# Optimization experiments

Hardware: AMD Instinct MI355X
Metric: run time of the kernel (lower is better)

## Reference

```python
import jax, jax.numpy as jnp
import numpy as np

C_SIZE = 512
DOWN = 8
W = C_SIZE // DOWN           # 64
REG = 10.0
N_ITER = 100                 # num_of_iter_in_ot

COOD = jnp.arange(0, C_SIZE, DOWN, dtype=jnp.float32) + DOWN / 2.0  # (W,)


def _cost_matrix(pts):
    # pts: (N,2) pixel coords -> squared L2 distance to every grid cell, (N, W*W)
    x = pts[:, 0:1]
    y = pts[:, 1:2]
    cood = COOD[None, :]
    x_dis = -2.0 * x * cood + x * x + cood * cood      # (N, W)
    y_dis = -2.0 * y * cood + y * y + cood * cood      # (N, W)
    dis = y_dis[:, :, None] + x_dis[:, None, :]        # (N, W, W): rows=y, cols=x
    return dis.reshape(pts.shape[0], -1)


def _asgd_semi_dual(a, b, M, idxs):
    # POT ot.stochastic.solve_semi_dual_entropic with method='asgd'.
    # a: (n,) target (point) weights; b: (m,) source (density) weights; M: (n, m).
    n, m = M.shape
    lr = 1.0 / jnp.max(a / REG)          # POT default lr
    log_b = jnp.log(b)

    def step(carry, xk):
        cur, ave = carry
        i, k = xk
        Mi = M[i]
        khi = jax.nn.softmax((cur - Mi) / REG + log_b)   # stable softmax
        cur = cur + (lr / jnp.sqrt(k)) * (b - khi)
        ave = cur / k + (1.0 - 1.0 / k) * ave
        return (cur, ave), None

    ks = jnp.arange(1, idxs.shape[0] + 1, dtype=jnp.float32)
    (_, beta), _ = jax.lax.scan(step, (jnp.zeros(m, M.dtype), jnp.zeros(m, M.dtype)), (idxs, ks))
    # c-transform: alpha_i = -reg * log sum_j exp((beta_j - M_ij)/reg) * b_j
    alpha = -REG * jax.scipy.special.logsumexp((beta[None, :] - M) / REG + log_b[None, :], axis=1)
    pi = jnp.exp((alpha[:, None] + beta[None, :] - M) / REG) * a[:, None] * b[None, :]
    return beta, pi


def _per_sample(normed, unnormed, pts, idxs):
    # normed, unnormed: (W, W); pts: (N, 2); idxs: (N_ITER,)
    n = pts.shape[0]
    a = jnp.full((n,), 1.0 / n, dtype=jnp.float32)
    dis = jax.lax.stop_gradient(_cost_matrix(pts))            # cupy path: no grad
    b = jax.lax.stop_gradient(normed.reshape(-1))             # src_prob detached
    beta, pi = _asgd_semi_dual(a, b, dis, idxs)
    beta = jax.lax.stop_gradient(beta)
    ot_obj = jnp.sum(normed.reshape(-1) * beta)
    src = jax.lax.stop_gradient(unnormed.reshape(-1))         # source_density detached
    sc = src.sum()
    denom = sc * sc + 1e-16
    im_grad = jax.lax.stop_gradient(sc / denom * beta - jnp.sum(src * beta) / denom)
    loss = jnp.sum(unnormed.reshape(-1) * im_grad)
    wd = jnp.sum(dis * jax.lax.stop_gradient(pi))
    return loss, wd, ot_obj


def setup_inputs() -> dict:
    key = jax.random.key(0)
    k1, k2 = jax.random.split(key, 2)
    unnormed = jax.random.uniform(k1, (16, 1, W, W), dtype=jnp.float32)
    normed = unnormed / unnormed.sum(axis=(1, 2, 3), keepdims=True)
    points = jax.random.uniform(k2, (16, 512, 2), dtype=jnp.float32) * C_SIZE
    return {"normed_density": normed, "unnormed_density": unnormed, "points": points}


def reference(normed_density, unnormed_density, points):
    B = normed_density.shape[0]
    # random coordinate indices for ASGD (constant, deterministic)
    idxs = jax.random.randint(jax.random.key(1), (B, N_ITER), 0, points.shape[1])
    loss, wd, ot_obj = jax.vmap(_per_sample)(
        normed_density[:, 0], unnormed_density[:, 0], points, idxs)
    return jnp.stack([loss.sum(), wd.sum(), ot_obj.sum()])
```

## Files before the change

### kernel.cpp

```cpp
#include <hip/hip_runtime.h>
#include <math.h>

#define NSAMP 16
#define NPTS  512
#define MDIM  4096
#define NIT   100

#define R0MAX 48


__device__ __forceinline__ int swz(int r, int c) {
  return r * 64 + (c ^ ((r & 1) << 4));
}

__device__ __forceinline__ void tf2x32(unsigned k0, unsigned k1,
                                       unsigned c0, unsigned c1,
                                       unsigned &o0, unsigned &o1)
{
  unsigned ks2 = k0 ^ k1 ^ 0x1BD11BDAu;
  unsigned x0 = c0 + k0, x1 = c1 + k1;
#define ROT(r) x0 += x1; x1 = (x1 << (r)) | (x1 >> (32 - (r))); x1 ^= x0;
#define G0 ROT(13) ROT(15) ROT(26) ROT(6)
#define G1 ROT(17) ROT(29) ROT(16) ROT(24)
  G0 x0 += k1;  x1 += ks2 + 1u;
  G1 x0 += ks2; x1 += k0  + 2u;
  G0 x0 += k0;  x1 += k1  + 3u;
  G1 x0 += k1;  x1 += ks2 + 4u;
  G0 x0 += ks2; x1 += k0  + 5u;
#undef G0
#undef G1
#undef ROT
  o0 = x0; o1 = x1;
}

__device__ __forceinline__ int rand_idx(int f)
{
  unsigned ka, kb, w0, w1;
  tf2x32(0u, 1u, 0u, 1u, ka, kb);
  tf2x32(ka, kb, 0u, (unsigned)f, w0, w1);
  return (int)((w0 ^ w1) & 511u);
}

template<int CTRL>
__device__ __forceinline__ float dpp_mv(float v, float id)
{
  return __int_as_float(__builtin_amdgcn_update_dpp(
      __float_as_int(id), __float_as_int(v), CTRL, 0xF, 0xF, false));
}

__device__ __forceinline__ float waveSum(float v)
{
  v += dpp_mv<0x111>(v, 0.0f);
  v += dpp_mv<0x112>(v, 0.0f);
  v += dpp_mv<0x114>(v, 0.0f);
  v += dpp_mv<0x118>(v, 0.0f);
  v += dpp_mv<0x142>(v, 0.0f);
  v += dpp_mv<0x143>(v, 0.0f);
  return __int_as_float(__builtin_amdgcn_readlane(__float_as_int(v), 63));
}

__global__ __launch_bounds__(1024) void kern_fused(
    const float *__restrict__ normed, const float *__restrict__ pts,
    float *__restrict__ out)
{
  const int s = blockIdx.x;
  const int t = threadIdx.x;
  const int v = t >> 6;
  const int L = t & 63;

  __shared__ float2 dav[MDIM];
  __shared__ float  barr[MDIM];
  __shared__ float2 pts2[NPTS];
  __shared__ float4 cstA[NIT + 4];
  __shared__ int2   cstB[NIT + 4];
  __shared__ float  spfin;
  __shared__ float  wdred[16], otred[16];

  #pragma unroll
  for (int l = 0; l < 4; ++l) {
    const int r = 4 * v + l;
    const float bv = normed[s * MDIM + r * 64 + L];
    const int idx = swz(r, L);
    dav[idx]  = make_float2(__logf(bv), 0.0f);
    barr[idx] = bv;
  }
  if (t < NPTS) pts2[t] = ((const float2 *)pts)[s * NPTS + t];
  if (t < NIT + 4) {
    const int kk = t < NIT ? t : (NIT - 1);
    const int idx = rand_idx(s * NIT + kk);
    const float2 p = ((const float2 *)pts)[s * NPTS + idx];
    const int rn = (int)floorf((p.y - 4.0f) * 0.125f + 0.5f);
    const int cn = (int)floorf((p.x - 4.0f) * 0.125f + 0.5f);
    int r0 = rn - 7; r0 = r0 < 0 ? 0 : (r0 > R0MAX ? R0MAX : r0);
    int c0 = cn - 7; c0 = c0 < 0 ? 0 : (c0 > R0MAX ? R0MAX : c0);
    const float kf    = (float)(kk + 1);
    const float step1 = 512.0f * __builtin_amdgcn_rsqf(kf);
    const float Pk    = step1 * (0.01f * (101.0f - kf));
    cstA[t] = make_float4(p.x - (float)(8 * c0 + 4),
                          p.y - (float)(8 * r0 + 4), step1, Pk);
    cstB[t] = make_int2(r0, c0);
  }
  __syncthreads();

  const int rbase = L >> 4;
  const int cbase = L & 15;
  const float fc8 = (float)(8 * cbase);
  const float fr8 = (float)(8 * rbase);

  if (t == 64) {
    float SPa = 0.0f;
    for (int k = 0; k < NIT; ++k) SPa += cstA[k].w;
    spfin = SPa;
  }
  if (v == 0) {
    float A = 0.0f;
    float4 cA = cstA[0];
    int2   cB = cstB[0];
    int j0 = swz(cB.x + rbase, cB.y + cbase);
    float2 c0v = dav[j0      ]; float b0v = barr[j0      ];
    float2 c1v = dav[j0 + 256]; float b1v = barr[j0 + 256];
    float2 c2v = dav[j0 + 512]; float b2v = barr[j0 + 512];
    float2 c3v = dav[j0 + 768]; float b3v = barr[j0 + 768];

    for (int k = 0; k < NIT; ++k) {
      const float4 cAn = cstA[k + 1];
      const int2   cBn = cstB[k + 1];

      const float dx  = cA.x - fc8;
      const float dxx = dx * dx;
      const float ty  = cA.y - fr8;
      const float e0 = __expf(fmaf(fmaf(ty,          ty,          dxx), -0.1f, fmaf(b0v, A, c0v.x)));
      const float e1 = __expf(fmaf(fmaf(ty - 32.0f, ty - 32.0f, dxx), -0.1f, fmaf(b1v, A, c1v.x)));
      const float e2 = __expf(fmaf(fmaf(ty - 64.0f, ty - 64.0f, dxx), -0.1f, fmaf(b2v, A, c2v.x)));
      const float e3 = __expf(fmaf(fmaf(ty - 96.0f, ty - 96.0f, dxx), -0.1f, fmaf(b3v, A, c3v.x)));

      const float S    = waveSum((e0 + e1) + (e2 + e3));
      const float invS = __builtin_amdgcn_rcpf(S);
      const float cD = cA.z * invS, cAv = cA.w * invS;

      c0v.x = fmaf(-cD, e0, c0v.x); c0v.y = fmaf(cAv, e0, c0v.y);
      c1v.x = fmaf(-cD, e1, c1v.x); c1v.y = fmaf(cAv, e1, c1v.y);
      c2v.x = fmaf(-cD, e2, c2v.x); c2v.y = fmaf(cAv, e2, c2v.y);
      c3v.x = fmaf(-cD, e3, c3v.x); c3v.y = fmaf(cAv, e3, c3v.y);
      dav[j0      ] = c0v;
      dav[j0 + 256] = c1v;
      dav[j0 + 512] = c2v;
      dav[j0 + 768] = c3v;

      A += cA.z;

      cA = cAn; cB = cBn;
      j0 = swz(cB.x + rbase, cB.y + cbase);
      c0v = dav[j0      ]; b0v = barr[j0      ];
      c1v = dav[j0 + 256]; b1v = barr[j0 + 256];
      c2v = dav[j0 + 512]; b2v = barr[j0 + 512];
      c3v = dav[j0 + 768]; b3v = barr[j0 + 768];
    }
  }
  __syncthreads();

  {
    const float SP = spfin;
    float p_ot = 0.0f;
    #pragma unroll
    for (int l = 0; l < 4; ++l) {
      const int idx = swz(4 * v + l, L);
      const float2 cd = dav[idx];
      const float bb  = barr[idx];
      const float tt  = fmaf(bb, SP, -cd.y);
      barr[idx] = tt + __logf(bb);
      p_ot = fmaf(bb, 10.0f * tt, p_ot);
    }
    p_ot = waveSum(p_ot);
    if (L == 0) otred[v] = p_ot;
  }
  __syncthreads();

  float wdacc = 0.0f;
  for (int g = 0; g < 8; ++g) {
    float pe[4], pq[4];
    #pragma unroll
    for (int i = 0; i < 4; ++i) {
      const int p = 32 * v + 4 * g + i;
      const float2 pt = pts2[p];
      const float x = pt.x, y = pt.y;
      const int rn = (int)floorf((y - 4.0f) * 0.125f + 0.5f);
      const int cn = (int)floorf((x - 4.0f) * 0.125f + 0.5f);
      int r0 = rn - 7; r0 = r0 < 0 ? 0 : (r0 > R0MAX ? R0MAX : r0);
      int c0 = cn - 7; c0 = c0 < 0 ? 0 : (c0 > R0MAX ? R0MAX : c0);
      const int rl = r0 + rbase;
      const int cl = c0 + cbase;
      const int j0 = swz(rl, cl);

      const float dx  = x - (float)(8 * cl + 4);
      const float dxx = dx * dx;
      const float ty  = y - (float)(8 * rl + 4);
      float spe = 0.0f, spq = 0.0f;
      #pragma unroll
      for (int q = 0; q < 4; ++q) {
        const float wv = barr[j0 + 256 * q];
        const float dy = ty - (float)(32 * q);
        const float qq = fmaf(dy, dy, dxx);
        const float e  = __expf(fmaf(qq, -0.1f, wv));
        spe += e;
        spq = fmaf(e, qq, spq);
      }
      pe[i] = spe; pq[i] = spq;
    }
    #pragma unroll
    for (int i = 0; i < 4; ++i) { pe[i] += dpp_mv<0x111>(pe[i], 0.0f); pq[i] += dpp_mv<0x111>(pq[i], 0.0f); }
    #pragma unroll
    for (int i = 0; i < 4; ++i) { pe[i] += dpp_mv<0x112>(pe[i], 0.0f); pq[i] += dpp_mv<0x112>(pq[i], 0.0f); }
    #pragma unroll
    for (int i = 0; i < 4; ++i) { pe[i] += dpp_mv<0x114>(pe[i], 0.0f); pq[i] += dpp_mv<0x114>(pq[i], 0.0f); }
    #pragma unroll
    for (int i = 0; i < 4; ++i) { pe[i] += dpp_mv<0x118>(pe[i], 0.0f); pq[i] += dpp_mv<0x118>(pq[i], 0.0f); }
    #pragma unroll
    for (int i = 0; i < 4; ++i) { pe[i] += dpp_mv<0x142>(pe[i], 0.0f); pq[i] += dpp_mv<0x142>(pq[i], 0.0f); }
    #pragma unroll
    for (int i = 0; i < 4; ++i) { pe[i] += dpp_mv<0x143>(pe[i], 0.0f); pq[i] += dpp_mv<0x143>(pq[i], 0.0f); }
    #pragma unroll
    for (int i = 0; i < 4; ++i) {
      const float PE = __int_as_float(__builtin_amdgcn_readlane(__float_as_int(pe[i]), 63));
      const float PQ = __int_as_float(__builtin_amdgcn_readlane(__float_as_int(pq[i]), 63));
      wdacc = fmaf(PQ, __builtin_amdgcn_rcpf(PE), wdacc);
    }
  }
  if (L == 0) wdred[v] = wdacc;
  __syncthreads();
  if (t == 0) {
    float wd = 0.0f, ot = 0.0f;
    #pragma unroll
    for (int i = 0; i < 16; ++i) { wd += wdred[i]; ot += otred[i]; }
    atomicAdd(&out[1], wd * (1.0f / 512.0f));
    atomicAdd(&out[2], ot);
  }
}

extern "C" void kernel_launch(void* const* d_in, const int* in_sizes, int n_in,
                              void* d_out, int out_size, void* d_ws, size_t ws_size,
                              hipStream_t stream)
{
  (void)in_sizes; (void)n_in; (void)out_size; (void)d_ws; (void)ws_size;
  const float *normed = (const float *)d_in[0];
  const float *pts    = (const float *)d_in[2];
  float *out = (float *)d_out;

  hipMemsetAsync(out, 0, 3 * sizeof(float), stream);
  kern_fused<<<dim3(NSAMP), dim3(1024), 0, stream>>>(normed, pts, out);
}
```

Baseline: 92.78 us.

## Batch disjoint-window ASGD iterations across waves with block barriers

Instead of running all 100 sequential ASGD updates on one wave, the kernel groups up to four consecutive iterations whose 32x32-region windows do not overlap and runs each on a separate wave. Because updates to disjoint regions commute, the batches execute in parallel with a __syncthreads between batches. A prefix-sum array of step sizes lets each wave know the running A value for its iteration. This adds a block-wide barrier per batch plus serial batch planning by one thread, which may cost more than the saved serial steps if windows often overlap.

```diff
diff --git a/kernel.cpp b/kernel.cpp
--- a/kernel.cpp
+++ b/kernel.cpp
@@ -8,9 +8,17 @@
 
 #define R0MAX 48
 
+#define MAXB 4
+
 
 __device__ __forceinline__ int swz(int r, int c) {
   return r * 64 + (c ^ ((r & 1) << 4));
+}
+
+__device__ __forceinline__ int wdisj(int2 a, int2 b) {
+  int dr = a.x - b.x; if (dr < 0) dr = -dr;
+  int dc = a.y - b.y; if (dc < 0) dc = -dc;
+  return (dr >= 16) | (dc >= 16);
 }
 
 __device__ __forceinline__ void tf2x32(unsigned k0, unsigned k1,
@@ -73,6 +81,11 @@
   __shared__ float2 pts2[NPTS];
   __shared__ float4 cstA[NIT + 4];
   __shared__ int2   cstB[NIT + 4];
+  __shared__ float  Aarr[NIT];
+  __shared__ int    lenb[NIT];
+  __shared__ int    bstart_s[NIT];
+  __shared__ int    bsize_s[NIT];
+  __shared__ int    nbat_s;
   __shared__ float  spfin;
   __shared__ float  wdred[16], otred[16];
 
@@ -102,62 +115,99 @@
   }
   __syncthreads();
 
+  if (t < NIT) {
+    const int2 w0 = cstB[t];
+    int e1 = 0, e2 = 0, e3 = 0;
+    if (t + 1 < NIT) {
+      const int2 w1 = cstB[t + 1];
+      e1 = wdisj(w0, w1);
+      if (e1 && t + 2 < NIT) {
+        const int2 w2 = cstB[t + 2];
+        e2 = wdisj(w0, w2) & wdisj(w1, w2);
+        if (e2 && t + 3 < NIT) {
+          const int2 w3 = cstB[t + 3];
+          e3 = wdisj(w0, w3) & wdisj(w1, w3) & wdisj(w2, w3);
+        }
+      }
+    }
+    lenb[t] = 1 + e1 + e2 + e3;
+  }
+  __syncthreads();
+
+  if (t == 0) {
+    int i = 0, b = 0;
+    while (i < NIT) {
+      bstart_s[b] = i;
+      const int Lb = lenb[i];
+      bsize_s[b] = Lb;
+      i += Lb;
+      ++b;
+    }
+    nbat_s = b;
+  } else if (t == 64) {
+    float A = 0.0f, SPa = 0.0f;
+    for (int k = 0; k < NIT; ++k) {
+      Aarr[k] = A;
+      A   += cstA[k].z;
+      SPa += cstA[k].w;
+    }
+    spfin = SPa;
+  }
+  __syncthreads();
+
   const int rbase = L >> 4;
   const int cbase = L & 15;
   const float fc8 = (float)(8 * cbase);
   const float fr8 = (float)(8 * rbase);
 
-  if (t == 64) {
-    float SPa = 0.0f;
-    for (int k = 0; k < NIT; ++k) SPa += cstA[k].w;
-    spfin = SPa;
-  }
-  if (v == 0) {
-    float A = 0.0f;
-    float4 cA = cstA[0];
-    int2   cB = cstB[0];
-    int j0 = swz(cB.x + rbase, cB.y + cbase);
-    float2 c0v = dav[j0      ]; float b0v = barr[j0      ];
-    float2 c1v = dav[j0 + 256]; float b1v = barr[j0 + 256];
-    float2 c2v = dav[j0 + 512]; float b2v = barr[j0 + 512];
-    float2 c3v = dav[j0 + 768]; float b3v = barr[j0 + 768];
-
-    for (int k = 0; k < NIT; ++k) {
-      const float4 cAn = cstA[k + 1];
-      const int2   cBn = cstB[k + 1];
-
-      const float dx  = cA.x - fc8;
-      const float dxx = dx * dx;
-      const float ty  = cA.y - fr8;
-      const float e0 = __expf(fmaf(fmaf(ty,          ty,          dxx), -0.1f, fmaf(b0v, A, c0v.x)));
-      const float e1 = __expf(fmaf(fmaf(ty - 32.0f, ty - 32.0f, dxx), -0.1f, fmaf(b1v, A, c1v.x)));
-      const float e2 = __expf(fmaf(fmaf(ty - 64.0f, ty - 64.0f, dxx), -0.1f, fmaf(b2v, A, c2v.x)));
-      const float e3 = __expf(fmaf(fmaf(ty - 96.0f, ty - 96.0f, dxx), -0.1f, fmaf(b3v, A, c3v.x)));
-
-      const float S    = waveSum((e0 + e1) + (e2 + e3));
-      const float invS = __builtin_amdgcn_rcpf(S);
-      const float cD = cA.z * invS, cAv = cA.w * invS;
-
-      c0v.x = fmaf(-cD, e0, c0v.x); c0v.y = fmaf(cAv, e0, c0v.y);
-      c1v.x = fmaf(-cD, e1, c1v.x); c1v.y = fmaf(cAv, e1, c1v.y);
-      c2v.x = fmaf(-cD, e2, c2v.x); c2v.y = fmaf(cAv, e2, c2v.y);
-      c3v.x = fmaf(-cD, e3, c3v.x); c3v.y = fmaf(cAv, e3, c3v.y);
-      dav[j0      ] = c0v;
-      dav[j0 + 256] = c1v;
-      dav[j0 + 512] = c2v;
-      dav[j0 + 768] = c3v;
-
-      A += cA.z;
-
-      cA = cAn; cB = cBn;
-      j0 = swz(cB.x + rbase, cB.y + cbase);
-      c0v = dav[j0      ]; b0v = barr[j0      ];
-      c1v = dav[j0 + 256]; b1v = barr[j0 + 256];
-      c2v = dav[j0 + 512]; b2v = barr[j0 + 512];
-      c3v = dav[j0 + 768]; b3v = barr[j0 + 768];
-    }
-  }
-  __syncthreads();
+  {
+    const int nb = nbat_s;
+    int   msize = bsize_s[0];
+    int   kme   = bstart_s[0] + (v < msize ? v : 0);
+    float4 cA = cstA[kme];
+    int2   cB = cstB[kme];
+    float  Ak = Aarr[kme];
+
+    for (int b = 0; b < nb; ++b) {
+      const int bn  = (b + 1 < nb) ? b + 1 : b;
+      const int sz2 = bsize_s[bn];
+      const int kn  = bstart_s[bn] + (v < sz2 ? v : 0);
+      const float4 cAn = cstA[kn];
+      const int2   cBn = cstB[kn];
+      const float  An  = Aarr[kn];
+
+      if (v < msize) {
+        const int j0 = swz(cB.x + rbase, cB.y + cbase);
+        float2 c0v = dav[j0      ]; const float b0v = barr[j0      ];
+        float2 c1v = dav[j0 + 256]; const float b1v = barr[j0 + 256];
+        float2 c2v = dav[j0 + 512]; const float b2v = barr[j0 + 512];
+        float2 c3v = dav[j0 + 768]; const float b3v = barr[j0 + 768];
+
+        const float dx  = cA.x - fc8;
+        const float dxx = dx * dx;
+        const float ty  = cA.y - fr8;
+        const float e0 = __expf(fmaf(fmaf(ty,          ty,          dxx), -0.1f, fmaf(b0v, Ak, c0v.x)));
+        const float e1 = __expf(fmaf(fmaf(ty - 32.0f, ty - 32.0f, dxx), -0.1f, fmaf(b1v, Ak, c1v.x)));
+        const float e2 = __expf(fmaf(fmaf(ty - 64.0f, ty - 64.0f, dxx), -0.1f, fmaf(b2v, Ak, c2v.x)));
+        const float e3 = __expf(fmaf(fmaf(ty - 96.0f, ty - 96.0f, dxx), -0.1f, fmaf(b3v, Ak, c3v.x)));
+
+        const float S    = waveSum((e0 + e1) + (e2 + e3));
+        const float invS = __builtin_amdgcn_rcpf(S);
+        const float cD = cA.z * invS, cAv = cA.w * invS;
+
+        c0v.x = fmaf(-cD, e0, c0v.x); c0v.y = fmaf(cAv, e0, c0v.y);
+        c1v.x = fmaf(-cD, e1, c1v.x); c1v.y = fmaf(cAv, e1, c1v.y);
+        c2v.x = fmaf(-cD, e2, c2v.x); c2v.y = fmaf(cAv, e2, c2v.y);
+        c3v.x = fmaf(-cD, e3, c3v.x); c3v.y = fmaf(cAv, e3, c3v.y);
+        dav[j0      ] = c0v;
+        dav[j0 + 256] = c1v;
+        dav[j0 + 512] = c2v;
+        dav[j0 + 768] = c3v;
+      }
+      __syncthreads();
+      msize = sz2; cA = cAn; cB = cBn; Ak = An;
+    }
+  }
 
   {
     const float SP = spfin;
```

Result: no change. 92.98 us (+0.2%).

## Split fused kernel into scan and parallel Wasserstein-distance kernels

Applied to the files above, without the earlier changes.

Splits the single per-sample kernel in two. The first runs the ASGD scan and writes the c-transform weights to workspace memory. The second spreads the Wasserstein-distance stage over eight blocks per sample (128 blocks) instead of one. The aim is to use many more compute units for the point-wise logsumexp phase, which previously ran on only 16 blocks. The cost is an extra kernel launch and a global-memory round trip for the weights.

```diff
diff --git a/kernel.cpp b/kernel.cpp
--- a/kernel.cpp
+++ b/kernel.cpp
@@ -59,9 +59,9 @@
   return __int_as_float(__builtin_amdgcn_readlane(__float_as_int(v), 63));
 }
 
-__global__ __launch_bounds__(1024) void kern_fused(
+__global__ __launch_bounds__(1024) void kern_scan(
     const float *__restrict__ normed, const float *__restrict__ pts,
-    float *__restrict__ out)
+    float *__restrict__ out, float *__restrict__ wglob)
 {
   const int s = blockIdx.x;
   const int t = threadIdx.x;
@@ -70,11 +70,10 @@
 
   __shared__ float2 dav[MDIM];
   __shared__ float  barr[MDIM];
-  __shared__ float2 pts2[NPTS];
   __shared__ float4 cstA[NIT + 4];
   __shared__ int2   cstB[NIT + 4];
   __shared__ float  spfin;
-  __shared__ float  wdred[16], otred[16];
+  __shared__ float  otred[16];
 
   #pragma unroll
   for (int l = 0; l < 4; ++l) {
@@ -84,7 +83,6 @@
     dav[idx]  = make_float2(__logf(bv), 0.0f);
     barr[idx] = bv;
   }
-  if (t < NPTS) pts2[t] = ((const float2 *)pts)[s * NPTS + t];
   if (t < NIT + 4) {
     const int kk = t < NIT ? t : (NIT - 1);
     const int idx = rand_idx(s * NIT + kk);
@@ -164,76 +162,107 @@
     float p_ot = 0.0f;
     #pragma unroll
     for (int l = 0; l < 4; ++l) {
-      const int idx = swz(4 * v + l, L);
+      const int r   = 4 * v + l;
+      const int idx = swz(r, L);
       const float2 cd = dav[idx];
       const float bb  = barr[idx];
       const float tt  = fmaf(bb, SP, -cd.y);
-      barr[idx] = tt + __logf(bb);
+      wglob[s * MDIM + r * 64 + L] = tt + __logf(bb);
       p_ot = fmaf(bb, 10.0f * tt, p_ot);
     }
     p_ot = waveSum(p_ot);
     if (L == 0) otred[v] = p_ot;
   }
   __syncthreads();
+  if (t == 0) {
+    float ot = 0.0f;
+    #pragma unroll
+    for (int i = 0; i < 16; ++i) ot += otred[i];
+    atomicAdd(&out[2], ot);
+  }
+}
+
+__global__ __launch_bounds__(1024) void kern_wd(
+    const float *__restrict__ pts, const float *__restrict__ wglob,
+    float *__restrict__ out)
+{
+  const int s = blockIdx.x >> 3;
+  const int q = blockIdx.x & 7;
+  const int t = threadIdx.x;
+  const int v = t >> 6;
+  const int L = t & 63;
+
+  __shared__ float  wlds[MDIM];
+  __shared__ float2 pts2[64];
+  __shared__ float  wdred[16];
+
+  #pragma unroll
+  for (int l = 0; l < 4; ++l) {
+    const int r = 4 * v + l;
+    wlds[swz(r, L)] = wglob[s * MDIM + r * 64 + L];
+  }
+  if (t < 64) pts2[t] = ((const float2 *)pts)[s * NPTS + 64 * q + t];
+  __syncthreads();
+
+  const int rbase = L >> 4;
+  const int cbase = L & 15;
+
+  float pe[4], pq[4];
+  #pragma unroll
+  for (int i = 0; i < 4; ++i) {
+    const int p = 4 * v + i;
+    const float2 pt = pts2[p];
+    const float x = pt.x, y = pt.y;
+    const int rn = (int)floorf((y - 4.0f) * 0.125f + 0.5f);
+    const int cn = (int)floorf((x - 4.0f) * 0.125f + 0.5f);
+    int r0 = rn - 7; r0 = r0 < 0 ? 0 : (r0 > R0MAX ? R0MAX : r0);
+    int c0 = cn - 7; c0 = c0 < 0 ? 0 : (c0 > R0MAX ? R0MAX : c0);
+    const int rl = r0 + rbase;
+    const int cl = c0 + cbase;
+    const int j0 = swz(rl, cl);
+
+    const float dx  = x - (float)(8 * cl + 4);
+    const float dxx = dx * dx;
+    const float ty  = y - (float)(8 * rl + 4);
+    float spe = 0.0f, spq = 0.0f;
+    #pragma unroll
+    for (int qq4 = 0; qq4 < 4; ++qq4) {
+      const float wv = wlds[j0 + 256 * qq4];
+      const float dy = ty - (float)(32 * qq4);
+      const float qq = fmaf(dy, dy, dxx);
+      const float e  = __expf(fmaf(qq, -0.1f, wv));
+      spe += e;
+      spq = fmaf(e, qq, spq);
+    }
+    pe[i] = spe; pq[i] = spq;
+  }
+  #pragma unroll
+  for (int i = 0; i < 4; ++i) { pe[i] += dpp_mv<0x111>(pe[i], 0.0f); pq[i] += dpp_mv<0x111>(pq[i], 0.0f); }
+  #pragma unroll
+  for (int i = 0; i < 4; ++i) { pe[i] += dpp_mv<0x112>(pe[i], 0.0f); pq[i] += dpp_mv<0x112>(pq[i], 0.0f); }
+  #pragma unroll
+  for (int i = 0; i < 4; ++i) { pe[i] += dpp_mv<0x114>(pe[i], 0.0f); pq[i] += dpp_mv<0x114>(pq[i], 0.0f); }
+  #pragma unroll
+  for (int i = 0; i < 4; ++i) { pe[i] += dpp_mv<0x118>(pe[i], 0.0f); pq[i] += dpp_mv<0x118>(pq[i], 0.0f); }
+  #pragma unroll
+  for (int i = 0; i < 4; ++i) { pe[i] += dpp_mv<0x142>(pe[i], 0.0f); pq[i] += dpp_mv<0x142>(pq[i], 0.0f); }
+  #pragma unroll
+  for (int i = 0; i < 4; ++i) { pe[i] += dpp_mv<0x143>(pe[i], 0.0f); pq[i] += dpp_mv<0x143>(pq[i], 0.0f); }
 
   float wdacc = 0.0f;
-  for (int g = 0; g < 8; ++g) {
-    float pe[4], pq[4];
-    #pragma unroll
-    for (int i = 0; i < 4; ++i) {
-      const int p = 32 * v + 4 * g + i;
-      const float2 pt = pts2[p];
-      const float x = pt.x, y = pt.y;
-      const int rn = (int)floorf((y - 4.0f) * 0.125f + 0.5f);
-      const int cn = (int)floorf((x - 4.0f) * 0.125f + 0.5f);
-      int r0 = rn - 7; r0 = r0 < 0 ? 0 : (r0 > R0MAX ? R0MAX : r0);
-      int c0 = cn - 7; c0 = c0 < 0 ? 0 : (c0 > R0MAX ? R0MAX : c0);
-      const int rl = r0 + rbase;
-      const int cl = c0 + cbase;
-      const int j0 = swz(rl, cl);
-
-      const float dx  = x - (float)(8 * cl + 4);
-      const float dxx = dx * dx;
-      const float ty  = y - (float)(8 * rl + 4);
-      float spe = 0.0f, spq = 0.0f;
-      #pragma unroll
-      for (int q = 0; q < 4; ++q) {
-        const float wv = barr[j0 + 256 * q];
-        const float dy = ty - (float)(32 * q);
-        const float qq = fmaf(dy, dy, dxx);
-        const float e  = __expf(fmaf(qq, -0.1f, wv));
-        spe += e;
-        spq = fmaf(e, qq, spq);
-      }
-      pe[i] = spe; pq[i] = spq;
-    }
-    #pragma unroll
-    for (int i = 0; i < 4; ++i) { pe[i] += dpp_mv<0x111>(pe[i], 0.0f); pq[i] += dpp_mv<0x111>(pq[i], 0.0f); }
-    #pragma unroll
-    for (int i = 0; i < 4; ++i) { pe[i] += dpp_mv<0x112>(pe[i], 0.0f); pq[i] += dpp_mv<0x112>(pq[i], 0.0f); }
-    #pragma unroll
-    for (int i = 0; i < 4; ++i) { pe[i] += dpp_mv<0x114>(pe[i], 0.0f); pq[i] += dpp_mv<0x114>(pq[i], 0.0f); }
-    #pragma unroll
-    for (int i = 0; i < 4; ++i) { pe[i] += dpp_mv<0x118>(pe[i], 0.0f); pq[i] += dpp_mv<0x118>(pq[i], 0.0f); }
-    #pragma unroll
-    for (int i = 0; i < 4; ++i) { pe[i] += dpp_mv<0x142>(pe[i], 0.0f); pq[i] += dpp_mv<0x142>(pq[i], 0.0f); }
-    #pragma unroll
-    for (int i = 0; i < 4; ++i) { pe[i] += dpp_mv<0x143>(pe[i], 0.0f); pq[i] += dpp_mv<0x143>(pq[i], 0.0f); }
-    #pragma unroll
-    for (int i = 0; i < 4; ++i) {
-      const float PE = __int_as_float(__builtin_amdgcn_readlane(__float_as_int(pe[i]), 63));
-      const float PQ = __int_as_float(__builtin_amdgcn_readlane(__float_as_int(pq[i]), 63));
-      wdacc = fmaf(PQ, __builtin_amdgcn_rcpf(PE), wdacc);
-    }
+  #pragma unroll
+  for (int i = 0; i < 4; ++i) {
+    const float PE = __int_as_float(__builtin_amdgcn_readlane(__float_as_int(pe[i]), 63));
+    const float PQ = __int_as_float(__builtin_amdgcn_readlane(__float_as_int(pq[i]), 63));
+    wdacc = fmaf(PQ, __builtin_amdgcn_rcpf(PE), wdacc);
   }
   if (L == 0) wdred[v] = wdacc;
   __syncthreads();
   if (t == 0) {
-    float wd = 0.0f, ot = 0.0f;
-    #pragma unroll
-    for (int i = 0; i < 16; ++i) { wd += wdred[i]; ot += otred[i]; }
+    float wd = 0.0f;
+    #pragma unroll
+    for (int i = 0; i < 16; ++i) wd += wdred[i];
     atomicAdd(&out[1], wd * (1.0f / 512.0f));
-    atomicAdd(&out[2], ot);
   }
 }
 
@@ -241,11 +270,13 @@
                               void* d_out, int out_size, void* d_ws, size_t ws_size,
                               hipStream_t stream)
 {
-  (void)in_sizes; (void)n_in; (void)out_size; (void)d_ws; (void)ws_size;
+  (void)in_sizes; (void)n_in; (void)out_size; (void)ws_size;
   const float *normed = (const float *)d_in[0];
   const float *pts    = (const float *)d_in[2];
-  float *out = (float *)d_out;
+  float *out   = (float *)d_out;
+  float *wglob = (float *)d_ws;
 
   hipMemsetAsync(out, 0, 3 * sizeof(float), stream);
-  kern_fused<<<dim3(NSAMP), dim3(1024), 0, stream>>>(normed, pts, out);
-}
+  kern_scan<<<dim3(NSAMP),     dim3(1024), 0, stream>>>(normed, pts, out, wglob);
+  kern_wd  <<<dim3(NSAMP * 8), dim3(1024), 0, stream>>>(pts, wglob, out);
+}
```

New measurement: 84.30 us. -9.1%, faster.
